# Performance work log

Measured on AMD Instinct MI355X. Metric: run time of the kernel, lower is better.

The kernel has to match this reference:

```python
import jax, jax.numpy as jnp
import numpy as np
import math

EMBED = 512
DIM2 = 768

def setup_inputs() -> dict:
    key = jax.random.key(0)
    ks = jax.random.split(key, 14)
    B, L1, L2 = 16, 2048, 1024
    s1 = 1.0 / math.sqrt(EMBED)
    s2 = 1.0 / math.sqrt(DIM2)
    inp = {
        'input_tensor1': jax.random.normal(ks[0], (B, EMBED, L1), jnp.float32),
        'input_tensor2': jax.random.normal(ks[1], (B, DIM2, L2), jnp.float32),
        # Linear params for modality 1 (512 -> 512)
        'Wq1': jax.random.normal(ks[2], (EMBED, EMBED), jnp.float32) * s1,
        'bq1': jnp.zeros((EMBED,), jnp.float32),
        'Wk1': jax.random.normal(ks[3], (EMBED, EMBED), jnp.float32) * s1,
        'bk1': jnp.zeros((EMBED,), jnp.float32),
        'Wv1': jax.random.normal(ks[4], (EMBED, EMBED), jnp.float32) * s1,
        'bv1': jnp.zeros((EMBED,), jnp.float32),
        # Linear params for modality 2 (768 -> 512)
        'Wq2': jax.random.normal(ks[5], (DIM2, EMBED), jnp.float32) * s2,
        'bq2': jnp.zeros((EMBED,), jnp.float32),
        'Wk2': jax.random.normal(ks[6], (DIM2, EMBED), jnp.float32) * s2,
        'bk2': jnp.zeros((EMBED,), jnp.float32),
        'Wv2': jax.random.normal(ks[7], (DIM2, EMBED), jnp.float32) * s2,
        'bv2': jnp.zeros((EMBED,), jnp.float32),
    }
    return inp


def reference(input_tensor1, input_tensor2,
              Wq1, bq1, Wk1, bk1, Wv1, bv1,
              Wq2, bq2, Wk2, bk2, Wv2, bv2):
    scale = 1.0 / math.sqrt(EMBED)
    # [B, C, L] -> [B, L, C]
    x1 = jnp.swapaxes(input_tensor1, 1, 2)  # [B, L1, 512]
    x2 = jnp.swapaxes(input_tensor2, 1, 2)  # [B, L2, 768]
    q1 = x1 @ Wq1 + bq1  # [B, L1, E]
    k1 = x1 @ Wk1 + bk1
    v1 = x1 @ Wv1 + bv1
    q2 = x2 @ Wq2 + bq2  # [B, L2, E]
    k2 = x2 @ Wk2 + bk2
    v2 = x2 @ Wv2 + bv2
    # direction 1: queries from modality 2 attend to modality 1
    scores1 = jnp.einsum('bif,bjf->bij', q2, k1) * scale  # [B, L2, L1]
    probs1 = jax.nn.sigmoid(scores1)
    ctx1 = jnp.einsum('bij,bjf->bif', probs1, v1)  # [B, L2, E]
    # direction 2: queries from modality 1 attend to modality 2
    scores2 = jnp.einsum('bif,bjf->bij', q1, k2) * scale  # [B, L1, L2]
    probs2 = jax.nn.sigmoid(scores2)
    ctx2 = jnp.einsum('bij,bjf->bif', probs2, v2)  # [B, L1, E]
    return (ctx2, probs2, ctx1, probs1)
```

## Files before the change

kernel.cpp:

```cpp
#include <hip/hip_runtime.h>
#include <hip/hip_bf16.h>

#define DEVFN __device__ __forceinline__

typedef __attribute__((ext_vector_type(4))) float f32x4;
typedef __attribute__((ext_vector_type(8))) short s16x8;
typedef __attribute__((ext_vector_type(2))) short s16x2;
typedef __attribute__((ext_vector_type(8))) __bf16 bf16x8;

union FragU { s16x8 s; bf16x8 b; };

DEVFN short f2bs(float x) {
  union { __hip_bfloat16 h; short s; } u;
  u.h = __float2bfloat16(x);
  return u.s;
}

DEVFN void gload16(const void* g, void* l) {
  __builtin_amdgcn_global_load_lds(
      (const __attribute__((address_space(1))) void*)g,
      (__attribute__((address_space(3))) void*)l, 16, 0, 0);
}

template <int N> DEVFN void waitcnt_vm() {
  if constexpr (N == 0) asm volatile("s_waitcnt vmcnt(0)" ::: "memory");
  else if constexpr (N == 3) asm volatile("s_waitcnt vmcnt(3)" ::: "memory");
  else if constexpr (N == 4) asm volatile("s_waitcnt vmcnt(4)" ::: "memory");
  else if constexpr (N == 6) asm volatile("s_waitcnt vmcnt(6)" ::: "memory");
  else if constexpr (N == 8) asm volatile("s_waitcnt vmcnt(8)" ::: "memory");
  else static_assert(N == 0, "unsupported vmcnt");
}

__global__ __launch_bounds__(256) void transpose_cvt(
    const float* __restrict__ in, short* __restrict__ out, int C, int L) {
  __shared__ float tile[64][33];
  const int l0 = blockIdx.x * 32, c0 = blockIdx.y * 64;
  const size_t base = (size_t)blockIdx.z * C * L;
  const int tx = threadIdx.x, ty = threadIdx.y;
#pragma unroll
  for (int i = ty; i < 64; i += 8)
    tile[i][tx] = in[base + (size_t)(c0 + i) * L + l0 + tx];
  __syncthreads();
#pragma unroll
  for (int i = ty; i < 32; i += 8) {
    s16x2 v;
    v[0] = f2bs(tile[2 * tx][i]);
    v[1] = f2bs(tile[2 * tx + 1][i]);
    *(s16x2*)&out[base + (size_t)(l0 + i) * C + c0 + 2 * tx] = v;
  }
}

__global__ __launch_bounds__(256) void prep_weights(
    const float* __restrict__ Wq1, const float* __restrict__ Wk1,
    const float* __restrict__ Wv1, const float* __restrict__ Wq2,
    const float* __restrict__ Wk2, const float* __restrict__ Wv2,
    short* wq1t, short* wk1t, short* wv1t,
    short* wq2t, short* wk2t, short* wv2t,
    const float* __restrict__ bq1, const float* __restrict__ bk1,
    const float* __restrict__ bq2, const float* __restrict__ bk2,
    float* b1c, float* b2c) {
  const int z = blockIdx.z;
  if (z == 6) {
    if (blockIdx.y != 0 || blockIdx.x >= 8) return;
    const int bx = blockIdx.x;
    const int tid = threadIdx.y * 32 + threadIdx.x;
    const int i = (bx & 3) * 256 + tid;
    const float* s = (bx < 4) ? ((i < 512) ? bq1 : bk1)
                              : ((i < 512) ? bq2 : bk2);
    float* d = (bx < 4) ? b1c : b2c;
    d[i] = s[i & 511];
    return;
  }
  const float* W; short* O; int C;
  switch (z) {
    case 0: W = Wq1; O = wq1t; C = 512; break;
    case 1: W = Wk1; O = wk1t; C = 512; break;
    case 2: W = Wv1; O = wv1t; C = 512; break;
    case 3: W = Wq2; O = wq2t; C = 768; break;
    case 4: W = Wk2; O = wk2t; C = 768; break;
    default: W = Wv2; O = wv2t; C = 768; break;
  }
  if (blockIdx.y * 64 >= (unsigned)C) return;
  const int L = 512;
  __shared__ float tile[64][33];
  const int l0 = blockIdx.x * 32, c0 = blockIdx.y * 64;
  const int tx = threadIdx.x, ty = threadIdx.y;
#pragma unroll
  for (int i = ty; i < 64; i += 8)
    tile[i][tx] = W[(size_t)(c0 + i) * L + l0 + tx];
  __syncthreads();
#pragma unroll
  for (int i = ty; i < 32; i += 8) {
    s16x2 v;
    v[0] = f2bs(tile[2 * tx][i]);
    v[1] = f2bs(tile[2 * tx + 1][i]);
    *(s16x2*)&O[(size_t)(l0 + i) * C + c0 + 2 * tx] = v;
  }
}

template <int OUTMODE, int BIASMODE, int MR>
__global__ __launch_bounds__(512, 2) void gemm8d(
    const short* __restrict__ A0, const short* __restrict__ B0,
    const float* __restrict__ bias0, void* __restrict__ C0,
    short* __restrict__ D0,
    int K0, int lda0, int ldb0, int ldc0,
    long long sA0, long long sB0, long long sC0,
    unsigned gx0, unsigned gy0, unsigned nb0,
    const short* __restrict__ A1, const short* __restrict__ B1,
    const float* __restrict__ bias1, void* __restrict__ C1,
    short* __restrict__ D1,
    int K1, int lda1, int ldb1, int ldc1,
    long long sA1, long long sB1, long long sC1,
    unsigned gx1, unsigned gy1,
    float scale) {
  constexpr int BM = MR * 32;
  constexpr int BN = 256;
  constexpr int LA = BM / 128;
  constexpr int LB = BN / 128;
  constexpr int LPT = LA + LB;
  constexpr int ABYTES = BM * 64;
  constexpr int BUFB = (BM + BN) * 64;
  constexpr int MH = MR / 2;
  __shared__ __align__(16) char smem[4 * BUFB];
  const int tid = threadIdx.x;
  const int lane = tid & 63, wid = tid >> 6;
  const int wm = wid >> 2, wn = wid & 3;

  const unsigned h = blockIdx.x;
  const bool sec = h >= nb0;
  const unsigned hh = sec ? h - nb0 : h;
  const unsigned nb = sec ? gridDim.x - nb0 : nb0;
  const unsigned gx = sec ? gx1 : gx0;
  const unsigned gy = sec ? gy1 : gy0;
  const short* Ap = sec ? A1 : A0;
  const short* Btp = sec ? B1 : B0;
  const float* bias = sec ? bias1 : bias0;
  void* Cptr = sec ? C1 : C0;
  short* C2p = sec ? D1 : D0;
  const int K = sec ? K1 : K0;
  const int lda = sec ? lda1 : lda0;
  const int ldb = sec ? ldb1 : ldb0;
  const int ldc = sec ? ldc1 : ldc0;
  const long long sA = sec ? sA1 : sA0;
  const long long sB = sec ? sB1 : sB0;
  const long long sC = sec ? sC1 : sC0;

  unsigned l = ((nb & 7u) == 0u) ? (hh & 7u) * (nb >> 3) + (hh >> 3) : hh;
  const unsigned bx = l % gx;
  const unsigned rem = l / gx;
  const unsigned by = rem % gy;
  const unsigned bz = rem / gy;

  const int zb = bz;
  const int m0 = by * BM, n0 = bx * BN;
  const char* Ab = (const char*)(Ap + (size_t)zb * sA);
  const char* Bb = (const char*)(Btp + (size_t)zb * sB);
  const size_t lda2 = (size_t)lda * 2, ldb2 = (size_t)ldb * 2;

  int s_r[2], s_cb[2];
#pragma unroll
  for (int j = 0; j < 2; ++j) {
    const int d = j * 8192 + tid * 16;
    const int line = d >> 7;
    s_r[j] = line * 2 + ((d >> 6) & 1);
    s_cb[j] = (d & 63) ^ ((line & 3) << 4);
  }

  f32x4 acc[MR][4] = {};
  const int frow = lane & 15, fkg = lane >> 4;

  int ra[MR], rb[4];
#pragma unroll
  for (int mf = 0; mf < MR; ++mf) {
    const int R = wm * (MR * 16) + mf * 16 + frow;
    ra[mf] = (R >> 1) * 128 + (R & 1) * 64 + ((fkg * 16) ^ (((R >> 1) & 3) << 4));
  }
#pragma unroll
  for (int nf = 0; nf < 4; ++nf) {
    const int R = wn * 64 + nf * 16 + frow;
    rb[nf] = (R >> 1) * 128 + (R & 1) * 64 + ((fkg * 16) ^ (((R >> 1) & 3) << 4));
  }

  const int NT = K >> 5;

#define STAGE_A(t)                                                       \
  {                                                                      \
    char* base_ = smem + ((t) & 3) * BUFB;                               \
    const size_t kb_ = (size_t)(t) * 64;                                 \
    _Pragma("unroll")                                                    \
    for (int j = 0; j < LA; ++j)                                         \
      gload16(Ab + (size_t)(m0 + s_r[j]) * lda2 + kb_ + s_cb[j],         \
              base_ + j * 8192 + tid * 16);                              \
  }
#define STAGE_B(t)                                                       \
  {                                                                      \
    char* base_ = smem + ((t) & 3) * BUFB + ABYTES;                      \
    const size_t kb_ = (size_t)(t) * 64;                                 \
    _Pragma("unroll")                                                    \
    for (int j = 0; j < LB; ++j)                                         \
      gload16(Bb + (size_t)(n0 + s_r[j]) * ldb2 + kb_ + s_cb[j],         \
              base_ + j * 8192 + tid * 16);                              \
  }

  STAGE_A(0); STAGE_B(0);
  STAGE_A(1); STAGE_B(1);
  STAGE_A(2); STAGE_B(2);
  waitcnt_vm<2 * LPT>();
  __builtin_amdgcn_sched_barrier(0);
  __builtin_amdgcn_s_barrier();
  __builtin_amdgcn_sched_barrier(0);

  for (int t = 0; t < NT; ++t) {
    const char* la = smem + (t & 3) * BUFB;
    const char* lb = la + ABYTES;
    FragU fa[MR], fb[4];
    if (t + 3 < NT) STAGE_A(t + 3);
#pragma unroll
    for (int mf = 0; mf < MH; ++mf) fa[mf].s = *(const s16x8*)(la + ra[mf]);
#pragma unroll
    for (int nf = 0; nf < 4; ++nf) fb[nf].s = *(const s16x8*)(lb + rb[nf]);
    __builtin_amdgcn_s_barrier();
    asm volatile("s_waitcnt lgkmcnt(0)" ::: "memory");
    __builtin_amdgcn_sched_barrier(0);
    __builtin_amdgcn_s_setprio(1);
#pragma unroll
    for (int mf = 0; mf < MH; ++mf)
#pragma unroll
      for (int nf = 0; nf < 4; ++nf)
        acc[mf][nf] = __builtin_amdgcn_mfma_f32_16x16x32_bf16(
            fa[mf].b, fb[nf].b, acc[mf][nf], 0, 0, 0);
    __builtin_amdgcn_s_setprio(0);
    __builtin_amdgcn_s_barrier();
    if (t + 3 < NT) STAGE_B(t + 3);
#pragma unroll
    for (int mf = MH; mf < MR; ++mf) fa[mf].s = *(const s16x8*)(la + ra[mf]);
    __builtin_amdgcn_s_barrier();
    asm volatile("s_waitcnt lgkmcnt(0)" ::: "memory");
    __builtin_amdgcn_sched_barrier(0);
    __builtin_amdgcn_s_setprio(1);
#pragma unroll
    for (int mf = MH; mf < MR; ++mf)
#pragma unroll
      for (int nf = 0; nf < 4; ++nf)
        acc[mf][nf] = __builtin_amdgcn_mfma_f32_16x16x32_bf16(
            fa[mf].b, fb[nf].b, acc[mf][nf], 0, 0, 0);
    __builtin_amdgcn_s_setprio(0);
    if (t + 3 < NT) {
      waitcnt_vm<2 * LPT>();
    } else if (t + 2 < NT) {
      waitcnt_vm<LPT>();
    } else if (t + 1 < NT) {
      waitcnt_vm<0>();
    } else {
      break;
    }
    __builtin_amdgcn_sched_barrier(0);
    __builtin_amdgcn_s_barrier();
    __builtin_amdgcn_sched_barrier(0);
  }
#undef STAGE_A
#undef STAGE_B

  const int rbase = (lane >> 4) * 4, cbase = lane & 15;
#pragma unroll
  for (int mf = 0; mf < MR; ++mf) {
#pragma unroll
    for (int nf = 0; nf < 4; ++nf) {
      const int gcol = n0 + wn * 64 + nf * 16 + cbase;
      float bn = (BIASMODE == 1) ? bias[gcol] : 0.f;
#pragma unroll
      for (int r = 0; r < 4; ++r) {
        const int grow = m0 + wm * (MR * 16) + mf * 16 + rbase + r;
        const size_t idx = (size_t)zb * sC + (size_t)grow * ldc + gcol;
        float v = acc[mf][nf][r];
        if constexpr (BIASMODE == 2) v += bias[grow]; else v += bn;
        if constexpr (OUTMODE == 0) {
          ((short*)Cptr)[idx] = f2bs(v);
        } else if constexpr (OUTMODE == 1) {
          __builtin_nontemporal_store(v, &((float*)Cptr)[idx]);
        } else if constexpr (OUTMODE == 2) {
          float p = 1.0f / (1.0f + __expf(-v * scale));
          __builtin_nontemporal_store(p, &((float*)Cptr)[idx]);
        } else {
          float p = 1.0f / (1.0f + __expf(-v * scale));
          __builtin_nontemporal_store(p, &((float*)Cptr)[idx]);
          C2p[idx] = f2bs(p);
        }
      }
    }
  }
}

template <int OUTMODE, int BIASMODE, int AF32>
__global__ __launch_bounds__(256) void gemm_bt(
    const void* __restrict__ Aptr, const short* __restrict__ Btp,
    const float* __restrict__ bias, void* __restrict__ Cptr,
    short* __restrict__ C2p,
    int K, int lda, int ldb, int ldc,
    long long sA, long long sB, long long sC, float scale) {
  __shared__ __align__(16) short lsA[128 * 64];
  __shared__ __align__(16) short lsB[128 * 64];
  const int tid = threadIdx.x;
  const int lane = tid & 63, wid = tid >> 6;
  const int zb = blockIdx.z;
  const int m0 = blockIdx.y * 128, n0 = blockIdx.x * 128;
  const short* Ab = AF32 ? nullptr : (const short*)Aptr + (size_t)zb * sA;
  const float* Af = AF32 ? (const float*)Aptr + (size_t)zb * sA : nullptr;
  const short* Bt = Btp + (size_t)zb * sB;

  f32x4 acc[4][4] = {};
  const int woffM = (wid >> 1) * 64, woffN = (wid & 1) * 64;
  const int frow = lane & 15, fkg = lane >> 4;

  for (int k0 = 0; k0 < K; k0 += 64) {
    if (k0) __syncthreads();
    if constexpr (!AF32) {
#pragma unroll
      for (int i = 0; i < 4; ++i) {
        const int f = i * 4096 + tid * 16;
        const int row = f >> 7, colb = f & 127;
        gload16((const char*)Ab + ((size_t)(m0 + row) * lda + k0) * 2 + colb,
                (char*)lsA + f);
      }
    } else {
#pragma unroll
      for (int i = 0; i < 8; ++i) {
        int f = tid + i * 256;
        int row = f >> 4, c4 = f & 15;
        f32x4 v = *(const f32x4*)&Af[(size_t)(m0 + row) * lda + k0 + c4 * 4];
        union { short s[4]; unsigned long long q; } cv;
#pragma unroll
        for (int j = 0; j < 4; ++j) cv.s[j] = f2bs(v[j]);
        *(unsigned long long*)&lsA[row * 64 + c4 * 4] = cv.q;
      }
    }
#pragma unroll
    for (int i = 0; i < 4; ++i) {
      const int f = i * 4096 + tid * 16;
      const int row = f >> 7, colb = f & 127;
      gload16((const char*)Bt + ((size_t)(n0 + row) * ldb + k0) * 2 + colb,
              (char*)lsB + f);
    }
    __syncthreads();
#pragma unroll
    for (int kk = 0; kk < 2; ++kk) {
      const int kb = kk * 32 + fkg * 8;
      FragU fa[4], fb[4];
#pragma unroll
      for (int mf = 0; mf < 4; ++mf)
        fa[mf].s = *(const s16x8*)&lsA[(woffM + mf * 16 + frow) * 64 + kb];
#pragma unroll
      for (int nf = 0; nf < 4; ++nf)
        fb[nf].s = *(const s16x8*)&lsB[(woffN + nf * 16 + frow) * 64 + kb];
#pragma unroll
      for (int mf = 0; mf < 4; ++mf)
#pragma unroll
        for (int nf = 0; nf < 4; ++nf)
          acc[mf][nf] = __builtin_amdgcn_mfma_f32_16x16x32_bf16(
              fa[mf].b, fb[nf].b, acc[mf][nf], 0, 0, 0);
    }
  }

  const int rbase = (lane >> 4) * 4, cbase = lane & 15;
#pragma unroll
  for (int mf = 0; mf < 4; ++mf) {
#pragma unroll
    for (int nf = 0; nf < 4; ++nf) {
      const int gcol = n0 + woffN + nf * 16 + cbase;
      float bn = (BIASMODE == 1) ? bias[gcol] : 0.f;
#pragma unroll
      for (int r = 0; r < 4; ++r) {
        const int grow = m0 + woffM + mf * 16 + rbase + r;
        const size_t idx = (size_t)zb * sC + (size_t)grow * ldc + gcol;
        float v = acc[mf][nf][r];
        if constexpr (BIASMODE == 2) v += bias[grow]; else v += bn;
        if constexpr (OUTMODE == 0) {
          ((short*)Cptr)[idx] = f2bs(v);
        } else if constexpr (OUTMODE == 1) {
          ((float*)Cptr)[idx] = v;
        } else if constexpr (OUTMODE == 2) {
          ((float*)Cptr)[idx] = 1.0f / (1.0f + __expf(-v * scale));
        } else {
          float p = 1.0f / (1.0f + __expf(-v * scale));
          ((float*)Cptr)[idx] = p;
          C2p[idx] = f2bs(p);
        }
      }
    }
  }
}

extern "C" void kernel_launch(void* const* d_in, const int* in_sizes, int n_in,
                              void* d_out, int out_size, void* d_ws, size_t ws_size,
                              hipStream_t stream) {
  const float* in1 = (const float*)d_in[0];
  const float* in2 = (const float*)d_in[1];
  const float* Wq1 = (const float*)d_in[2];  const float* bq1 = (const float*)d_in[3];
  const float* Wk1 = (const float*)d_in[4];  const float* bk1 = (const float*)d_in[5];
  const float* Wv1 = (const float*)d_in[6];  const float* bv1 = (const float*)d_in[7];
  const float* Wq2 = (const float*)d_in[8];  const float* bq2 = (const float*)d_in[9];
  const float* Wk2 = (const float*)d_in[10]; const float* bk2 = (const float*)d_in[11];
  const float* Wv2 = (const float*)d_in[12]; const float* bv2 = (const float*)d_in[13];

  float* out = (float*)d_out;
  float* ctx2   = out;
  float* probs2 = out + (size_t)16 * 2048 * 512;
  float* ctx1   = probs2 + (size_t)16 * 2048 * 1024;
  float* probs1 = ctx1 + (size_t)16 * 1024 * 512;

  char* ws = (char*)d_ws;
  constexpr size_t O_WQ1T = 0;
  constexpr size_t O_WK1T = O_WQ1T + (size_t)512 * 512 * 2;
  constexpr size_t O_WV1T = O_WK1T + (size_t)512 * 512 * 2;
  constexpr size_t O_WQ2T = O_WV1T + (size_t)512 * 512 * 2;
  constexpr size_t O_WK2T = O_WQ2T + (size_t)768 * 512 * 2;
  constexpr size_t O_WV2T = O_WK2T + (size_t)768 * 512 * 2;
  constexpr size_t O_B1   = O_WV2T + (size_t)768 * 512 * 2;
  constexpr size_t O_B2   = O_B1 + 4096;
  constexpr size_t O_QK1  = O_B2 + 4096;
  constexpr size_t O_V1T  = O_QK1 + (size_t)32768 * 1024 * 2;
  constexpr size_t O_QK2  = O_V1T + (size_t)16 * 512 * 2048 * 2;
  constexpr size_t O_V2T  = O_QK2 + (size_t)16384 * 1024 * 2;
  constexpr size_t O_X1B  = O_V2T + (size_t)16 * 512 * 1024 * 2;
  constexpr size_t O_X2B  = O_X1B + (size_t)32768 * 512 * 2;
  constexpr size_t O_PB1  = O_X2B + (size_t)16384 * 768 * 2;
  constexpr size_t O_PB2  = O_PB1 + (size_t)16 * 1024 * 2048 * 2;
  constexpr size_t NEED_A = O_PB2 + (size_t)16 * 2048 * 1024 * 2;
  constexpr size_t NEED_B = O_PB1;

  short* wq1t = (short*)(ws + O_WQ1T);
  short* wk1t = (short*)(ws + O_WK1T);
  short* wv1t = (short*)(ws + O_WV1T);
  short* wq2t = (short*)(ws + O_WQ2T);
  short* wk2t = (short*)(ws + O_WK2T);
  short* wv2t = (short*)(ws + O_WV2T);
  float* b1c  = (float*)(ws + O_B1);
  float* b2c  = (float*)(ws + O_B2);
  short* qk1  = (short*)(ws + O_QK1);
  short* v1t  = (short*)(ws + O_V1T);
  short* qk2  = (short*)(ws + O_QK2);
  short* v2t  = (short*)(ws + O_V2T);
  short* x1b  = (short*)(ws + O_X1B);
  short* x2b  = (short*)(ws + O_X2B);
  short* pb1  = (short*)(ws + O_PB1);
  short* pb2  = (short*)(ws + O_PB2);

  const bool tierA = ws_size >= NEED_A;
  const bool tierB = ws_size >= NEED_B;
  if (!tierB) { x1b = (short*)probs1; x2b = (short*)probs2; }

  dim3 blk256(256), blk512(512);
  dim3 blkT(32, 8);

  transpose_cvt<<<dim3(64, 8, 16), blkT, 0, stream>>>(in1, x1b, 512, 2048);
  transpose_cvt<<<dim3(32, 12, 16), blkT, 0, stream>>>(in2, x2b, 768, 1024);
  prep_weights<<<dim3(16, 12, 7), blkT, 0, stream>>>(
      Wq1, Wk1, Wv1, Wq2, Wk2, Wv2, wq1t, wk1t, wv1t, wq2t, wk2t, wv2t,
      bq1, bk1, bq2, bk2, b1c, b2c);

  const float scale = 0.04419417382415922f;
  const short* q1p = qk1;
  const short* k1p = qk1 + 512;
  const short* q2p = qk2;
  const short* k2p = qk2 + 512;

  if (tierA) {
    gemm8d<0, 1, 8><<<dim3(768), blk512, 0, stream>>>(
        x1b, wq1t, b1c, qk1, nullptr, 512, 512, 512, 1024, 0, 0, 0,
        4u, 128u, 512u,
        x2b, wq2t, b2c, qk2, nullptr, 768, 768, 768, 1024, 0, 0, 0,
        4u, 64u, 1.f);
    gemm8d<0, 2, 4><<<dim3(768), blk512, 0, stream>>>(
        wv1t, x1b, bv1, v1t, nullptr, 512, 512, 512, 2048,
        0, (long long)2048 * 512, (long long)512 * 2048,
        8u, 4u, 512u,
        wv2t, x2b, bv2, v2t, nullptr, 768, 768, 768, 1024,
        0, (long long)1024 * 768, (long long)512 * 1024,
        4u, 4u, 1.f);
    gemm8d<3, 0, 8><<<dim3(1024), blk512, 0, stream>>>(
        q2p, k1p, nullptr, probs1, pb1, 512, 1024, 1024, 2048,
        (long long)1024 * 1024, (long long)2048 * 1024, (long long)1024 * 2048,
        8u, 4u, 512u,
        q1p, k2p, nullptr, probs2, pb2, 512, 1024, 1024, 1024,
        (long long)2048 * 1024, (long long)1024 * 1024, (long long)2048 * 1024,
        4u, 8u, scale);
    gemm8d<1, 0, 4><<<dim3(768), blk512, 0, stream>>>(
        pb1, v1t, nullptr, ctx1, nullptr, 2048, 2048, 2048, 512,
        (long long)1024 * 2048, (long long)512 * 2048, (long long)1024 * 512,
        2u, 8u, 256u,
        pb2, v2t, nullptr, ctx2, nullptr, 1024, 1024, 1024, 512,
        (long long)2048 * 1024, (long long)512 * 1024, (long long)2048 * 512,
        2u, 16u, 1.f);
  } else {
    gemm_bt<0, 1, 0><<<dim3(8, 256, 1), blk256, 0, stream>>>(
        x1b, wq1t, b1c, qk1, nullptr, 512, 512, 512, 1024, 0, 0, 0, 1.f);
    gemm_bt<0, 1, 0><<<dim3(8, 128, 1), blk256, 0, stream>>>(
        x2b, wq2t, b2c, qk2, nullptr, 768, 768, 768, 1024, 0, 0, 0, 1.f);
    gemm_bt<0, 2, 0><<<dim3(16, 4, 16), blk256, 0, stream>>>(
        wv1t, x1b, bv1, v1t, nullptr, 512, 512, 512, 2048,
        0, (long long)2048 * 512, (long long)512 * 2048, 1.f);
    gemm_bt<0, 2, 0><<<dim3(8, 4, 16), blk256, 0, stream>>>(
        wv2t, x2b, bv2, v2t, nullptr, 768, 768, 768, 1024,
        0, (long long)1024 * 768, (long long)512 * 1024, 1.f);
    gemm_bt<2, 0, 0><<<dim3(16, 8, 16), blk256, 0, stream>>>(
        q2p, k1p, nullptr, probs1, nullptr, 512, 1024, 1024, 2048,
        (long long)1024 * 1024, (long long)2048 * 1024, (long long)1024 * 2048, scale);
    gemm_bt<2, 0, 0><<<dim3(8, 16, 16), blk256, 0, stream>>>(
        q1p, k2p, nullptr, probs2, nullptr, 512, 1024, 1024, 1024,
        (long long)2048 * 1024, (long long)1024 * 1024, (long long)2048 * 1024, scale);
    gemm_bt<1, 0, 1><<<dim3(4, 8, 16), blk256, 0, stream>>>(
        probs1, v1t, nullptr, ctx1, nullptr, 2048, 2048, 2048, 512,
        (long long)1024 * 2048, (long long)512 * 2048, (long long)1024 * 512, 1.f);
    gemm_bt<1, 0, 1><<<dim3(4, 16, 16), blk256, 0, stream>>>(
        probs2, v2t, nullptr, ctx2, nullptr, 1024, 1024, 1024, 512,
        (long long)2048 * 1024, (long long)512 * 1024, (long long)2048 * 512, 1.f);
  }
}
```

Measured before the change: 440.3 us.

## Fuse sigmoid-attention score and context GEMMs into one flash-style kernel

Replaces the separate score GEMM (which wrote fp32 probs plus a bf16 copy to workspace) and the probs·V GEMM with a single fused kernel. Each 128-row query tile loops over key tiles, computes the sigmoid scores, writes fp32 probs to the output, keeps the bf16 probs in LDS, and immediately accumulates P·V into a 128x512 register accumulator. This removes the bf16 probs round trip through HBM and one launch. In exchange only 384 blocks run, each holding a large accumulator with 128 KB of LDS, which lowers occupancy and parallelism and serializes the two GEMM phases inside each block.

```diff
diff --git a/kernel.cpp b/kernel.cpp
--- a/kernel.cpp
+++ b/kernel.cpp
@@ -2,6 +2,7 @@
 #include <hip/hip_bf16.h>
 
 #define DEVFN __device__ __forceinline__
+#define SB __builtin_amdgcn_sched_barrier(0)
 
 typedef __attribute__((ext_vector_type(4))) float f32x4;
 typedef __attribute__((ext_vector_type(8))) short s16x8;
@@ -24,6 +25,7 @@
 
 template <int N> DEVFN void waitcnt_vm() {
   if constexpr (N == 0) asm volatile("s_waitcnt vmcnt(0)" ::: "memory");
+  else if constexpr (N == 2) asm volatile("s_waitcnt vmcnt(2)" ::: "memory");
   else if constexpr (N == 3) asm volatile("s_waitcnt vmcnt(3)" ::: "memory");
   else if constexpr (N == 4) asm volatile("s_waitcnt vmcnt(4)" ::: "memory");
   else if constexpr (N == 6) asm volatile("s_waitcnt vmcnt(6)" ::: "memory");
@@ -101,18 +103,15 @@
 template <int OUTMODE, int BIASMODE, int MR>
 __global__ __launch_bounds__(512, 2) void gemm8d(
     const short* __restrict__ A0, const short* __restrict__ B0,
-    const float* __restrict__ bias0, void* __restrict__ C0,
-    short* __restrict__ D0,
+    const float* __restrict__ bias0, void* __restrict__ C0, short* __restrict__ D0,
     int K0, int lda0, int ldb0, int ldc0,
     long long sA0, long long sB0, long long sC0,
     unsigned gx0, unsigned gy0, unsigned nb0,
     const short* __restrict__ A1, const short* __restrict__ B1,
-    const float* __restrict__ bias1, void* __restrict__ C1,
-    short* __restrict__ D1,
+    const float* __restrict__ bias1, void* __restrict__ C1, short* __restrict__ D1,
     int K1, int lda1, int ldb1, int ldc1,
     long long sA1, long long sB1, long long sC1,
-    unsigned gx1, unsigned gy1,
-    float scale) {
+    unsigned gx1, unsigned gy1, float scale) {
   constexpr int BM = MR * 32;
   constexpr int BN = 256;
   constexpr int LA = BM / 128;
@@ -206,9 +205,7 @@
   STAGE_A(1); STAGE_B(1);
   STAGE_A(2); STAGE_B(2);
   waitcnt_vm<2 * LPT>();
-  __builtin_amdgcn_sched_barrier(0);
-  __builtin_amdgcn_s_barrier();
-  __builtin_amdgcn_sched_barrier(0);
+  SB; __builtin_amdgcn_s_barrier(); SB;
 
   for (int t = 0; t < NT; ++t) {
     const char* la = smem + (t & 3) * BUFB;
@@ -221,7 +218,7 @@
     for (int nf = 0; nf < 4; ++nf) fb[nf].s = *(const s16x8*)(lb + rb[nf]);
     __builtin_amdgcn_s_barrier();
     asm volatile("s_waitcnt lgkmcnt(0)" ::: "memory");
-    __builtin_amdgcn_sched_barrier(0);
+    SB;
     __builtin_amdgcn_s_setprio(1);
 #pragma unroll
     for (int mf = 0; mf < MH; ++mf)
@@ -236,7 +233,7 @@
     for (int mf = MH; mf < MR; ++mf) fa[mf].s = *(const s16x8*)(la + ra[mf]);
     __builtin_amdgcn_s_barrier();
     asm volatile("s_waitcnt lgkmcnt(0)" ::: "memory");
-    __builtin_amdgcn_sched_barrier(0);
+    SB;
     __builtin_amdgcn_s_setprio(1);
 #pragma unroll
     for (int mf = MH; mf < MR; ++mf)
@@ -254,9 +251,7 @@
     } else {
       break;
     }
-    __builtin_amdgcn_sched_barrier(0);
-    __builtin_amdgcn_s_barrier();
-    __builtin_amdgcn_sched_barrier(0);
+    SB; __builtin_amdgcn_s_barrier(); SB;
   }
 #undef STAGE_A
 #undef STAGE_B
@@ -291,6 +286,204 @@
   }
 }
 
+__global__ __launch_bounds__(512, 2) void fused_sattn(
+    const short* __restrict__ Q0, const short* __restrict__ K0,
+    const short* __restrict__ V0, float* __restrict__ P0, float* __restrict__ C0,
+    int LK0, long long sQ0, long long sK0, long long sV0, long long sP0,
+    long long sC0, unsigned mt0, unsigned nb0,
+    const short* __restrict__ Q1, const short* __restrict__ K1,
+    const short* __restrict__ V1, float* __restrict__ P1, float* __restrict__ C1,
+    int LK1, long long sQ1, long long sK1, long long sV1, long long sP1,
+    long long sC1, unsigned mt1, float scale) {
+  constexpr int PBASE = 49152;
+  constexpr int VBASE = 81920;
+  __shared__ __align__(16) char smem[131072];
+  const int tid = threadIdx.x;
+  const int lane = tid & 63, wid = tid >> 6;
+  const int wm = wid >> 2, wn = wid & 3;
+  const int frow = lane & 15, fkg = lane >> 4;
+
+  const unsigned h = blockIdx.x;
+  const bool sec = h >= nb0;
+  const unsigned hh = sec ? h - nb0 : h;
+  const unsigned nb = sec ? gridDim.x - nb0 : nb0;
+  const unsigned mt = sec ? mt1 : mt0;
+  const short* Qp = sec ? Q1 : Q0;
+  const short* Kp = sec ? K1 : K0;
+  const short* Vp = sec ? V1 : V0;
+  float* Pp = sec ? P1 : P0;
+  float* Cp = sec ? C1 : C0;
+  const int LK = sec ? LK1 : LK0;
+  const long long sQ = sec ? sQ1 : sQ0;
+  const long long sK = sec ? sK1 : sK0;
+  const long long sV = sec ? sV1 : sV0;
+  const long long sP = sec ? sP1 : sP0;
+  const long long sC = sec ? sC1 : sC0;
+
+  unsigned l = ((nb & 7u) == 0u) ? (hh & 7u) * (nb >> 3) + (hh >> 3) : hh;
+  const unsigned by = l % mt;
+  const unsigned bz = l / mt;
+  const int m0 = by * 128;
+  const char* Qb = (const char*)(Qp + (size_t)bz * sQ);
+  const char* Kb = (const char*)(Kp + (size_t)bz * sK);
+  const char* Vb = (const char*)(Vp + (size_t)bz * sV);
+  float* Pg = Pp + (size_t)bz * sP;
+  float* Cg = Cp + (size_t)bz * sC;
+  const int NJ = LK >> 7;
+  const size_t ldv2 = (size_t)LK * 2;
+
+  int s_r, s_cb;
+  { int d = tid * 16; int line = d >> 7;
+    s_r = line * 2 + ((d >> 6) & 1); s_cb = (d & 63) ^ ((line & 3) << 4); }
+  int s_r2[2], s_cb2[2];
+#pragma unroll
+  for (int jj = 0; jj < 2; ++jj) {
+    int d = jj * 8192 + tid * 16; int line = d >> 7;
+    s_r2[jj] = line * 2 + ((d >> 6) & 1); s_cb2[jj] = (d & 63) ^ ((line & 3) << 4);
+  }
+
+  int raq[4], rbk[2], rbv[4], rap[4];
+#pragma unroll
+  for (int mf = 0; mf < 4; ++mf) {
+    const int R = wm * 64 + mf * 16 + frow;
+    raq[mf] = (R >> 1) * 128 + (R & 1) * 64 + ((fkg * 16) ^ (((R >> 1) & 3) << 4));
+    rap[mf] = PBASE + R * 256 + (((R & 7) << 4));
+  }
+#pragma unroll
+  for (int nf = 0; nf < 2; ++nf) {
+    const int R = wn * 32 + nf * 16 + frow;
+    rbk[nf] = 8192 + (R >> 1) * 128 + (R & 1) * 64 + ((fkg * 16) ^ (((R >> 1) & 3) << 4));
+  }
+#pragma unroll
+  for (int nf = 0; nf < 4; ++nf) {
+    const int R = wn * 64 + nf * 16 + frow;
+    rbv[nf] = (R >> 1) * 128 + (R & 1) * 64 + ((fkg * 16) ^ (((R >> 1) & 3) << 4));
+  }
+  const int pswz = fkg * 16;
+
+#define STAGE_S(ks, j0v)                                                   \
+  {                                                                        \
+    char* b_ = smem + ((ks) % 3) * 16384;                                  \
+    gload16(Qb + (size_t)(m0 + s_r) * 2048 + (ks) * 64 + s_cb,             \
+            b_ + tid * 16);                                                \
+    gload16(Kb + (size_t)((j0v) + s_r) * 2048 + (ks) * 64 + s_cb,          \
+            b_ + 8192 + tid * 16);                                         \
+  }
+#define STAGE_V(c, j0v)                                                    \
+  {                                                                        \
+    char* b_ = smem + VBASE + ((c) % 3) * 16384;                           \
+    _Pragma("unroll")                                                      \
+    for (int jj = 0; jj < 2; ++jj)                                         \
+      gload16(Vb + (size_t)(((c) >> 2) * 256 + s_r2[jj]) * ldv2 +          \
+                  (size_t)(j0v) * 2 + ((c) & 3) * 64 + s_cb2[jj],          \
+              b_ + jj * 8192 + tid * 16);                                  \
+  }
+
+  f32x4 accc[4][8] = {};
+  const int rbase = (lane >> 4) * 4, cbase = lane & 15;
+
+  STAGE_S(0, 0); STAGE_S(1, 0);
+
+  for (int jt = 0; jt < NJ; ++jt) {
+    const int j0 = jt * 128;
+    waitcnt_vm<2>();
+    SB; __builtin_amdgcn_s_barrier(); SB;
+    f32x4 accs[4][2] = {};
+#pragma unroll 4
+    for (int ks = 0; ks < 16; ++ks) {
+      if (ks < 14) STAGE_S(ks + 2, j0);
+      const char* bp = smem + (ks % 3) * 16384;
+      FragU fq[4], fk[2];
+#pragma unroll
+      for (int mf = 0; mf < 4; ++mf) fq[mf].s = *(const s16x8*)(bp + raq[mf]);
+#pragma unroll
+      for (int nf = 0; nf < 2; ++nf) fk[nf].s = *(const s16x8*)(bp + rbk[nf]);
+      asm volatile("s_waitcnt lgkmcnt(0)" ::: "memory");
+      SB;
+      __builtin_amdgcn_s_setprio(1);
+#pragma unroll
+      for (int mf = 0; mf < 4; ++mf)
+#pragma unroll
+        for (int nf = 0; nf < 2; ++nf)
+          accs[mf][nf] = __builtin_amdgcn_mfma_f32_16x16x32_bf16(
+              fq[mf].b, fk[nf].b, accs[mf][nf], 0, 0, 0);
+      __builtin_amdgcn_s_setprio(0);
+      if (ks < 14) waitcnt_vm<2>();
+      else if (ks == 14) waitcnt_vm<0>();
+      else break;
+      SB; __builtin_amdgcn_s_barrier(); SB;
+    }
+#pragma unroll
+    for (int mf = 0; mf < 4; ++mf)
+#pragma unroll
+      for (int nf = 0; nf < 2; ++nf)
+#pragma unroll
+        for (int r = 0; r < 4; ++r) {
+          const float p = 1.0f / (1.0f + __expf(-accs[mf][nf][r] * scale));
+          const int row = wm * 64 + mf * 16 + rbase + r;
+          const int col = wn * 32 + nf * 16 + cbase;
+          __builtin_nontemporal_store(
+              p, &Pg[(size_t)(m0 + row) * LK + j0 + col]);
+          *(short*)(smem + PBASE + row * 256 +
+                    ((2 * col) ^ ((row & 7) << 4))) = f2bs(p);
+        }
+    STAGE_V(0, j0); STAGE_V(1, j0);
+    SB;
+    asm volatile("s_waitcnt lgkmcnt(0)" ::: "memory");
+    __builtin_amdgcn_s_barrier(); SB;
+    const bool pre = (jt + 1 < NJ);
+#pragma unroll
+    for (int c = 0; c < 8; ++c) {
+      if (c < 6) STAGE_V(c + 2, j0);
+      if (c == 5 && pre) { STAGE_S(0, j0 + 128); STAGE_S(1, j0 + 128); }
+      const int q = c & 3, hf = c >> 2;
+      const char* vb = smem + VBASE + (c % 3) * 16384;
+      FragU pa[4], vv[4];
+#pragma unroll
+      for (int mf = 0; mf < 4; ++mf)
+        pa[mf].s = *(const s16x8*)(smem + (rap[mf] ^ (q * 64 + pswz)));
+#pragma unroll
+      for (int nf = 0; nf < 4; ++nf) vv[nf].s = *(const s16x8*)(vb + rbv[nf]);
+      asm volatile("s_waitcnt lgkmcnt(0)" ::: "memory");
+      SB;
+      __builtin_amdgcn_s_setprio(1);
+#pragma unroll
+      for (int mf = 0; mf < 4; ++mf)
+#pragma unroll
+        for (int nf = 0; nf < 4; ++nf)
+          accc[mf][hf * 4 + nf] = __builtin_amdgcn_mfma_f32_16x16x32_bf16(
+              pa[mf].b, vv[nf].b, accc[mf][hf * 4 + nf], 0, 0, 0);
+      __builtin_amdgcn_s_setprio(0);
+      if (c < 5) {
+        waitcnt_vm<2>();
+      } else if (c == 5) {
+        if (pre) waitcnt_vm<6>(); else waitcnt_vm<2>();
+      } else if (c == 6) {
+        if (pre) waitcnt_vm<4>(); else waitcnt_vm<0>();
+      } else {
+        break;
+      }
+      SB; __builtin_amdgcn_s_barrier(); SB;
+    }
+    SB; __builtin_amdgcn_s_barrier(); SB;
+  }
+#undef STAGE_S
+#undef STAGE_V
+
+#pragma unroll
+  for (int mf = 0; mf < 4; ++mf)
+#pragma unroll
+    for (int g = 0; g < 8; ++g) {
+      const int gcol = (g >> 2) * 256 + wn * 64 + (g & 3) * 16 + cbase;
+#pragma unroll
+      for (int r = 0; r < 4; ++r) {
+        const int grow = m0 + wm * 64 + mf * 16 + rbase + r;
+        __builtin_nontemporal_store(
+            accc[mf][g][r], &Cg[(size_t)grow * 512 + gcol]);
+      }
+    }
+}
+
 template <int OUTMODE, int BIASMODE, int AF32>
 __global__ __launch_bounds__(256) void gemm_bt(
     const void* __restrict__ Aptr, const short* __restrict__ Btp,
@@ -423,10 +616,7 @@
   constexpr size_t O_V2T  = O_QK2 + (size_t)16384 * 1024 * 2;
   constexpr size_t O_X1B  = O_V2T + (size_t)16 * 512 * 1024 * 2;
   constexpr size_t O_X2B  = O_X1B + (size_t)32768 * 512 * 2;
-  constexpr size_t O_PB1  = O_X2B + (size_t)16384 * 768 * 2;
-  constexpr size_t O_PB2  = O_PB1 + (size_t)16 * 1024 * 2048 * 2;
-  constexpr size_t NEED_A = O_PB2 + (size_t)16 * 2048 * 1024 * 2;
-  constexpr size_t NEED_B = O_PB1;
+  constexpr size_t NEED_B = O_X2B + (size_t)16384 * 768 * 2;
 
   short* wq1t = (short*)(ws + O_WQ1T);
   short* wk1t = (short*)(ws + O_WK1T);
@@ -442,12 +632,9 @@
   short* v2t  = (short*)(ws + O_V2T);
   short* x1b  = (short*)(ws + O_X1B);
   short* x2b  = (short*)(ws + O_X2B);
-  short* pb1  = (short*)(ws + O_PB1);
-  short* pb2  = (short*)(ws + O_PB2);
-
-  const bool tierA = ws_size >= NEED_A;
-  const bool tierB = ws_size >= NEED_B;
-  if (!tierB) { x1b = (short*)probs1; x2b = (short*)probs2; }
+
+  const bool tierA = ws_size >= NEED_B;
+  if (!tierA) { x1b = (short*)probs1; x2b = (short*)probs2; }
 
   dim3 blk256(256), blk512(512);
   dim3 blkT(32, 8);
@@ -477,20 +664,14 @@
         wv2t, x2b, bv2, v2t, nullptr, 768, 768, 768, 1024,
         0, (long long)1024 * 768, (long long)512 * 1024,
         4u, 4u, 1.f);
-    gemm8d<3, 0, 8><<<dim3(1024), blk512, 0, stream>>>(
-        q2p, k1p, nullptr, probs1, pb1, 512, 1024, 1024, 2048,
-        (long long)1024 * 1024, (long long)2048 * 1024, (long long)1024 * 2048,
-        8u, 4u, 512u,
-        q1p, k2p, nullptr, probs2, pb2, 512, 1024, 1024, 1024,
-        (long long)2048 * 1024, (long long)1024 * 1024, (long long)2048 * 1024,
-        4u, 8u, scale);
-    gemm8d<1, 0, 4><<<dim3(768), blk512, 0, stream>>>(
-        pb1, v1t, nullptr, ctx1, nullptr, 2048, 2048, 2048, 512,
-        (long long)1024 * 2048, (long long)512 * 2048, (long long)1024 * 512,
-        2u, 8u, 256u,
-        pb2, v2t, nullptr, ctx2, nullptr, 1024, 1024, 1024, 512,
-        (long long)2048 * 1024, (long long)512 * 1024, (long long)2048 * 512,
-        2u, 16u, 1.f);
+    fused_sattn<<<dim3(384), blk512, 0, stream>>>(
+        q2p, k1p, v1t, probs1, ctx1, 2048,
+        (long long)1024 * 1024, (long long)2048 * 1024, (long long)512 * 2048,
+        (long long)1024 * 2048, (long long)1024 * 512, 8u, 128u,
+        q1p, k2p, v2t, probs2, ctx2, 1024,
+        (long long)2048 * 1024, (long long)1024 * 1024, (long long)512 * 1024,
+        (long long)2048 * 1024, (long long)2048 * 512, 16u,
+        scale);
   } else {
     gemm_bt<0, 1, 0><<<dim3(8, 256, 1), blk256, 0, stream>>>(
         x1b, wq1t, b1c, qk1, nullptr, 512, 512, 512, 1024, 0, 0, 0, 1.f);
```

Result: slower. 495.2 us (+12.5%).

## Merge QK and V projection GEMMs into one four-problem grouped launch

Applied to the files above, without the earlier changes.

Adds a gemm8q kernel that takes four GEMM problem descriptors and dispatches each block to one of them by block index. The QK projections for both modalities and the V projections run in a single 1152-block launch instead of two separate launches. The V projections now use 256-row M tiles (MR=8) instead of 128, which halves the V block count. This removes one launch and the tail idle time between the two projection kernels, and raises per-block reuse for the V GEMMs. The cost is runtime branching on bias mode and a larger kernel-argument block.

```diff
diff --git a/kernel.cpp b/kernel.cpp
--- a/kernel.cpp
+++ b/kernel.cpp
@@ -2,6 +2,7 @@
 #include <hip/hip_bf16.h>
 
 #define DEVFN __device__ __forceinline__
+#define SB __builtin_amdgcn_sched_barrier(0)
 
 typedef __attribute__((ext_vector_type(4))) float f32x4;
 typedef __attribute__((ext_vector_type(8))) short s16x8;
@@ -24,6 +25,7 @@
 
 template <int N> DEVFN void waitcnt_vm() {
   if constexpr (N == 0) asm volatile("s_waitcnt vmcnt(0)" ::: "memory");
+  else if constexpr (N == 2) asm volatile("s_waitcnt vmcnt(2)" ::: "memory");
   else if constexpr (N == 3) asm volatile("s_waitcnt vmcnt(3)" ::: "memory");
   else if constexpr (N == 4) asm volatile("s_waitcnt vmcnt(4)" ::: "memory");
   else if constexpr (N == 6) asm volatile("s_waitcnt vmcnt(6)" ::: "memory");
@@ -98,21 +100,177 @@
   }
 }
 
+struct GArg {
+  const short* A; const short* B; const float* bias; short* C;
+  int K, lda, ldb, ldc;
+  long long sA, sB, sC;
+  unsigned gx, gy, nb;
+  int bm;
+};
+
+__global__ __launch_bounds__(512, 2) void gemm8q(
+    GArg g0, GArg g1, GArg g2, GArg g3) {
+  constexpr int MR = 8;
+  constexpr int BM = 256, BN = 256;
+  constexpr int LA = 2, LB = 2, LPT = 4;
+  constexpr int ABYTES = BM * 64;
+  constexpr int BUFB = (BM + BN) * 64;
+  constexpr int MH = MR / 2;
+  __shared__ __align__(16) char smem[4 * BUFB];
+  const int tid = threadIdx.x;
+  const int lane = tid & 63, wid = tid >> 6;
+  const int wm = wid >> 2, wn = wid & 3;
+
+  const unsigned h = blockIdx.x;
+  GArg ga; unsigned hh;
+  const unsigned b0 = g0.nb, b1 = b0 + g1.nb, b2 = b1 + g2.nb;
+  if (h < b0)      { ga = g0; hh = h; }
+  else if (h < b1) { ga = g1; hh = h - b0; }
+  else if (h < b2) { ga = g2; hh = h - b1; }
+  else             { ga = g3; hh = h - b2; }
+
+  const unsigned nb = ga.nb;
+  unsigned l = (hh & 7u) * (nb >> 3) + (hh >> 3);
+  const unsigned bx = l % ga.gx;
+  const unsigned rem = l / ga.gx;
+  const unsigned by = rem % ga.gy;
+  const unsigned bz = rem / ga.gy;
+
+  const int m0 = by * BM, n0 = bx * BN;
+  const char* Ab = (const char*)(ga.A + (size_t)bz * ga.sA);
+  const char* Bb = (const char*)(ga.B + (size_t)bz * ga.sB);
+  const size_t lda2 = (size_t)ga.lda * 2, ldb2 = (size_t)ga.ldb * 2;
+
+  int s_r[2], s_cb[2];
+#pragma unroll
+  for (int j = 0; j < 2; ++j) {
+    const int d = j * 8192 + tid * 16;
+    const int line = d >> 7;
+    s_r[j] = line * 2 + ((d >> 6) & 1);
+    s_cb[j] = (d & 63) ^ ((line & 3) << 4);
+  }
+
+  f32x4 acc[MR][4] = {};
+  const int frow = lane & 15, fkg = lane >> 4;
+
+  int ra[MR], rb[4];
+#pragma unroll
+  for (int mf = 0; mf < MR; ++mf) {
+    const int R = wm * (MR * 16) + mf * 16 + frow;
+    ra[mf] = (R >> 1) * 128 + (R & 1) * 64 + ((fkg * 16) ^ (((R >> 1) & 3) << 4));
+  }
+#pragma unroll
+  for (int nf = 0; nf < 4; ++nf) {
+    const int R = wn * 64 + nf * 16 + frow;
+    rb[nf] = (R >> 1) * 128 + (R & 1) * 64 + ((fkg * 16) ^ (((R >> 1) & 3) << 4));
+  }
+
+  const int NT = ga.K >> 5;
+
+#define STAGE_A(t)                                                       \
+  {                                                                      \
+    char* base_ = smem + ((t) & 3) * BUFB;                               \
+    const size_t kb_ = (size_t)(t) * 64;                                 \
+    _Pragma("unroll")                                                    \
+    for (int j = 0; j < LA; ++j)                                         \
+      gload16(Ab + (size_t)(m0 + s_r[j]) * lda2 + kb_ + s_cb[j],         \
+              base_ + j * 8192 + tid * 16);                              \
+  }
+#define STAGE_B(t)                                                       \
+  {                                                                      \
+    char* base_ = smem + ((t) & 3) * BUFB + ABYTES;                      \
+    const size_t kb_ = (size_t)(t) * 64;                                 \
+    _Pragma("unroll")                                                    \
+    for (int j = 0; j < LB; ++j)                                         \
+      gload16(Bb + (size_t)(n0 + s_r[j]) * ldb2 + kb_ + s_cb[j],         \
+              base_ + j * 8192 + tid * 16);                              \
+  }
+
+  STAGE_A(0); STAGE_B(0);
+  STAGE_A(1); STAGE_B(1);
+  STAGE_A(2); STAGE_B(2);
+  waitcnt_vm<2 * LPT>();
+  SB; __builtin_amdgcn_s_barrier(); SB;
+
+  for (int t = 0; t < NT; ++t) {
+    const char* la = smem + (t & 3) * BUFB;
+    const char* lb = la + ABYTES;
+    FragU fa[MR], fb[4];
+    if (t + 3 < NT) STAGE_A(t + 3);
+#pragma unroll
+    for (int mf = 0; mf < MH; ++mf) fa[mf].s = *(const s16x8*)(la + ra[mf]);
+#pragma unroll
+    for (int nf = 0; nf < 4; ++nf) fb[nf].s = *(const s16x8*)(lb + rb[nf]);
+    __builtin_amdgcn_s_barrier();
+    asm volatile("s_waitcnt lgkmcnt(0)" ::: "memory");
+    SB;
+    __builtin_amdgcn_s_setprio(1);
+#pragma unroll
+    for (int mf = 0; mf < MH; ++mf)
+#pragma unroll
+      for (int nf = 0; nf < 4; ++nf)
+        acc[mf][nf] = __builtin_amdgcn_mfma_f32_16x16x32_bf16(
+            fa[mf].b, fb[nf].b, acc[mf][nf], 0, 0, 0);
+    __builtin_amdgcn_s_setprio(0);
+    __builtin_amdgcn_s_barrier();
+    if (t + 3 < NT) STAGE_B(t + 3);
+#pragma unroll
+    for (int mf = MH; mf < MR; ++mf) fa[mf].s = *(const s16x8*)(la + ra[mf]);
+    __builtin_amdgcn_s_barrier();
+    asm volatile("s_waitcnt lgkmcnt(0)" ::: "memory");
+    SB;
+    __builtin_amdgcn_s_setprio(1);
+#pragma unroll
+    for (int mf = MH; mf < MR; ++mf)
+#pragma unroll
+      for (int nf = 0; nf < 4; ++nf)
+        acc[mf][nf] = __builtin_amdgcn_mfma_f32_16x16x32_bf16(
+            fa[mf].b, fb[nf].b, acc[mf][nf], 0, 0, 0);
+    __builtin_amdgcn_s_setprio(0);
+    if (t + 3 < NT) {
+      waitcnt_vm<2 * LPT>();
+    } else if (t + 2 < NT) {
+      waitcnt_vm<LPT>();
+    } else if (t + 1 < NT) {
+      waitcnt_vm<0>();
+    } else {
+      break;
+    }
+    SB; __builtin_amdgcn_s_barrier(); SB;
+  }
+#undef STAGE_A
+#undef STAGE_B
+
+  const int rbase = (lane >> 4) * 4, cbase = lane & 15;
+#pragma unroll
+  for (int mf = 0; mf < MR; ++mf) {
+#pragma unroll
+    for (int nf = 0; nf < 4; ++nf) {
+      const int gcol = n0 + wn * 64 + nf * 16 + cbase;
+      const float bn = (ga.bm == 1) ? ga.bias[gcol] : 0.f;
+#pragma unroll
+      for (int r = 0; r < 4; ++r) {
+        const int grow = m0 + wm * (MR * 16) + mf * 16 + rbase + r;
+        float v = acc[mf][nf][r] + bn;
+        if (ga.bm == 2) v += ga.bias[grow];
+        ga.C[(size_t)bz * ga.sC + (size_t)grow * ga.ldc + gcol] = f2bs(v);
+      }
+    }
+  }
+}
+
 template <int OUTMODE, int BIASMODE, int MR>
 __global__ __launch_bounds__(512, 2) void gemm8d(
     const short* __restrict__ A0, const short* __restrict__ B0,
-    const float* __restrict__ bias0, void* __restrict__ C0,
-    short* __restrict__ D0,
+    const float* __restrict__ bias0, void* __restrict__ C0, short* __restrict__ D0,
     int K0, int lda0, int ldb0, int ldc0,
     long long sA0, long long sB0, long long sC0,
     unsigned gx0, unsigned gy0, unsigned nb0,
     const short* __restrict__ A1, const short* __restrict__ B1,
-    const float* __restrict__ bias1, void* __restrict__ C1,
-    short* __restrict__ D1,
+    const float* __restrict__ bias1, void* __restrict__ C1, short* __restrict__ D1,
     int K1, int lda1, int ldb1, int ldc1,
     long long sA1, long long sB1, long long sC1,
-    unsigned gx1, unsigned gy1,
-    float scale) {
+    unsigned gx1, unsigned gy1, float scale) {
   constexpr int BM = MR * 32;
   constexpr int BN = 256;
   constexpr int LA = BM / 128;
@@ -206,9 +364,7 @@
   STAGE_A(1); STAGE_B(1);
   STAGE_A(2); STAGE_B(2);
   waitcnt_vm<2 * LPT>();
-  __builtin_amdgcn_sched_barrier(0);
-  __builtin_amdgcn_s_barrier();
-  __builtin_amdgcn_sched_barrier(0);
+  SB; __builtin_amdgcn_s_barrier(); SB;
 
   for (int t = 0; t < NT; ++t) {
     const char* la = smem + (t & 3) * BUFB;
@@ -221,7 +377,7 @@
     for (int nf = 0; nf < 4; ++nf) fb[nf].s = *(const s16x8*)(lb + rb[nf]);
     __builtin_amdgcn_s_barrier();
     asm volatile("s_waitcnt lgkmcnt(0)" ::: "memory");
-    __builtin_amdgcn_sched_barrier(0);
+    SB;
     __builtin_amdgcn_s_setprio(1);
 #pragma unroll
     for (int mf = 0; mf < MH; ++mf)
@@ -236,7 +392,7 @@
     for (int mf = MH; mf < MR; ++mf) fa[mf].s = *(const s16x8*)(la + ra[mf]);
     __builtin_amdgcn_s_barrier();
     asm volatile("s_waitcnt lgkmcnt(0)" ::: "memory");
-    __builtin_amdgcn_sched_barrier(0);
+    SB;
     __builtin_amdgcn_s_setprio(1);
 #pragma unroll
     for (int mf = MH; mf < MR; ++mf)
@@ -254,9 +410,7 @@
     } else {
       break;
     }
-    __builtin_amdgcn_sched_barrier(0);
-    __builtin_amdgcn_s_barrier();
-    __builtin_amdgcn_sched_barrier(0);
+    SB; __builtin_amdgcn_s_barrier(); SB;
   }
 #undef STAGE_A
 #undef STAGE_B
@@ -465,18 +619,15 @@
   const short* k2p = qk2 + 512;
 
   if (tierA) {
-    gemm8d<0, 1, 8><<<dim3(768), blk512, 0, stream>>>(
-        x1b, wq1t, b1c, qk1, nullptr, 512, 512, 512, 1024, 0, 0, 0,
-        4u, 128u, 512u,
-        x2b, wq2t, b2c, qk2, nullptr, 768, 768, 768, 1024, 0, 0, 0,
-        4u, 64u, 1.f);
-    gemm8d<0, 2, 4><<<dim3(768), blk512, 0, stream>>>(
-        wv1t, x1b, bv1, v1t, nullptr, 512, 512, 512, 2048,
-        0, (long long)2048 * 512, (long long)512 * 2048,
-        8u, 4u, 512u,
-        wv2t, x2b, bv2, v2t, nullptr, 768, 768, 768, 1024,
-        0, (long long)1024 * 768, (long long)512 * 1024,
-        4u, 4u, 1.f);
+    GArg a0{x1b, wq1t, b1c, qk1, 512, 512, 512, 1024,
+            0, 0, 0, 4u, 128u, 512u, 1};
+    GArg a1{x2b, wq2t, b2c, qk2, 768, 768, 768, 1024,
+            0, 0, 0, 4u, 64u, 256u, 1};
+    GArg a2{wv1t, x1b, bv1, v1t, 512, 512, 512, 2048,
+            0, (long long)2048 * 512, (long long)512 * 2048, 8u, 2u, 256u, 2};
+    GArg a3{wv2t, x2b, bv2, v2t, 768, 768, 768, 1024,
+            0, (long long)1024 * 768, (long long)512 * 1024, 4u, 2u, 128u, 2};
+    gemm8q<<<dim3(1152), blk512, 0, stream>>>(a0, a1, a2, a3);
     gemm8d<3, 0, 8><<<dim3(1024), blk512, 0, stream>>>(
         q2p, k1p, nullptr, probs1, pb1, 512, 1024, 1024, 2048,
         (long long)1024 * 1024, (long long)2048 * 1024, (long long)1024 * 2048,
```

Result: slower. 470.3 us (+6.8%).
